# Kernel optimization log

Hardware: AMD Instinct MI355X
Metric: run time of the kernel (lower is better)

## Reference

```python
import jax, jax.numpy as jnp
from jax import lax
import numpy as np

S = 3600  # spatial_size from scn.InputLayer
B = 1     # batch
P = 200000
NEG = jnp.float32(-1e30)


def setup_inputs() -> dict:
    key = jax.random.key(0)
    ks = jax.random.split(key, 10)
    coords = jax.random.randint(ks[0], (P, 2), 0, S, dtype=jnp.int32)
    features = jax.random.normal(ks[1], (P, 1), jnp.float32)
    w1 = jax.random.normal(ks[2], (5, 5, 1, 10), jnp.float32) * 0.2
    w2 = jax.random.normal(ks[3], (5, 5, 10, 64), jnp.float32) * 0.06
    w3 = jax.random.normal(ks[4], (5, 5, 64, 128), jnp.float32) * 0.025
    w4 = jax.random.normal(ks[5], (5, 5, 128, 256), jnp.float32) * 0.018
    fc1_w = jax.random.normal(ks[6], (256 * 9 * 9, 32), jnp.float32) * 0.01
    fc1_b = jax.random.normal(ks[7], (32,), jnp.float32) * 0.01
    fc2_w = jax.random.normal(ks[8], (32, 5), jnp.float32) * 0.1
    fc2_b = jax.random.normal(ks[9], (5,), jnp.float32) * 0.01
    return dict(coords=coords, features=features, w1=w1, w2=w2, w3=w3, w4=w4,
                fc1_w=fc1_w, fc1_b=fc1_b, fc2_w=fc2_w, fc2_b=fc2_b)


def _subm_conv(x, mask, w):
    # Submanifold conv == dense SAME conv on zero-filled grid, output kept
    # only at active sites (inactive inputs are exactly zero by construction).
    y = lax.conv_general_dilated(x, w, (1, 1), 'SAME',
                                 dimension_numbers=('NHWC', 'HWIO', 'NHWC'))
    return y * mask


def _sparse_maxpool(x, mask, k):
    # scn.MaxPooling: max over ACTIVE sites in each window; output site is
    # active iff any input site in the window is active, else feature = 0.
    neg = jnp.where(mask > 0, x, NEG)
    y = lax.reduce_window(neg, NEG, lax.max, (1, k, k, 1), (1, k, k, 1), 'VALID')
    new_mask = lax.reduce_window(mask, jnp.float32(0), lax.max,
                                 (1, k, k, 1), (1, k, k, 1), 'VALID')
    return jnp.where(new_mask > 0, y, 0.0), new_mask


def reference(coords, features, w1, w2, w3, w4, fc1_w, fc1_b, fc2_w, fc2_b):
    # scn.InputLayer: scatter sparse (coord, feature) pairs onto the grid
    x = jnp.zeros((B, S, S, 1), jnp.float32).at[0, coords[:, 0], coords[:, 1], :].add(features)
    mask = jnp.zeros((B, S, S, 1), jnp.float32).at[0, coords[:, 0], coords[:, 1], :].set(1.0)

    x = jax.nn.elu(_subm_conv(x, mask, w1))
    x, mask = _sparse_maxpool(x, mask, 5)   # 3600 -> 720
    x = jax.nn.elu(_subm_conv(x, mask, w2))
    x, mask = _sparse_maxpool(x, mask, 5)   # 720 -> 144
    x = jax.nn.elu(_subm_conv(x, mask, w3))
    x, mask = _sparse_maxpool(x, mask, 4)   # 144 -> 36
    x = jax.nn.elu(_subm_conv(x, mask, w4))
    x, mask = _sparse_maxpool(x, mask, 4)   # 36 -> 9

    # SparseToDense -> (B, 256, 9, 9), then view(-1, 256*9*9) in NCHW order
    h = x.transpose(0, 3, 1, 2).reshape(B, 256 * 9 * 9)
    h = jax.nn.elu(h @ fc1_w + fc1_b)
    logits = h @ fc2_w + fc2_b
    return jax.nn.softmax(logits, axis=1)
```

## Files before the change

### kernel.cpp

```cpp
#include <hip/hip_runtime.h>
#include <math.h>

#define S0 3600
#define S1 720
#define S2 144
#define S3 36
#define S4 9
#define NEGF (-1e30f)

static constexpr size_t OFF_X0  = 0;
static constexpr size_t OFF_M0B = (size_t)S0 * S0 * 4;
static constexpr size_t OFF_H1  = OFF_M0B + 1620000;
static constexpr size_t OFF_Y1H = OFF_H1 + 128;
static constexpr size_t OFF_M1  = OFF_Y1H + (size_t)S1 * S1 * 16 * 2;
static constexpr size_t OFF_M2  = 1330000;
static constexpr size_t OFF_Y3  = OFF_M2 + 20736;
static constexpr size_t OFF_M3  = OFF_Y3 + (size_t)S3 * S3 * 128 * 4;
static constexpr size_t OFF_Y4  = OFF_M3 + 1296;
static constexpr size_t OFF_Y2H = 13000000;
static constexpr size_t OFF_W3H = 18400000;
static constexpr size_t OFF_W2H = 19240000;
static constexpr size_t OFF_W4H = 19400000;

typedef __attribute__((ext_vector_type(8))) short bf16x8;
typedef __attribute__((ext_vector_type(4))) float f32x4;

__device__ __forceinline__ float eluf(float x) { return x > 0.f ? x : expm1f(x); }
__device__ __forceinline__ unsigned short f2bf(float f) {
    unsigned u = __float_as_uint(f);
    unsigned r = u + 0x7FFFu + ((u >> 16) & 1u);
    return (unsigned short)(r >> 16);
}
__device__ __forceinline__ float bf2f(unsigned short h) {
    return __uint_as_float((unsigned)h << 16);
}

__global__ __launch_bounds__(256) void k_zero(const int* __restrict__ coords,
                                              float* __restrict__ x0, int P) {
    int i = blockIdx.x * 256 + threadIdx.x;
    if (i >= P) return;
    x0[coords[2 * i] * S0 + coords[2 * i + 1]] = 0.f;
}

__global__ __launch_bounds__(256) void k_scatter(const int* __restrict__ coords,
                                                 const float* __restrict__ feats,
                                                 float* __restrict__ x0,
                                                 unsigned* __restrict__ m0b, int P) {
    int i = blockIdx.x * 256 + threadIdx.x;
    if (i >= P) return;
    int r = coords[2 * i], c = coords[2 * i + 1];
    int idx = r * S0 + c;
    atomicAdd(&x0[idx], feats[i]);
    atomicOr(&m0b[idx >> 5], 1u << (idx & 31));
}

__global__ __launch_bounds__(256) void k_l1(const float* __restrict__ x0,
                                            const unsigned* __restrict__ m0b,
                                            const float* __restrict__ w1,
                                            unsigned short* __restrict__ y1h,
                                            unsigned char* __restrict__ m1) {
    __shared__ float w1s[250];
    int tid = threadIdx.x;
    if (tid < 250) w1s[tid] = w1[tid];
    __syncthreads();
    int t = blockIdx.x * 256 + tid;
    int pr = t / S1, pc = t % S1;
    int r0 = pr * 5 - 2, c0 = pc * 5 - 2;
    unsigned rows[9];
#pragma unroll
    for (int rr = 0; rr < 9; rr++) {
        unsigned bits = 0;
        int gr = r0 + rr;
        if (gr >= 0 && gr < S0) {
            int cs = c0 < 0 ? 0 : c0;
            int ce = c0 + 8 > S0 - 1 ? S0 - 1 : c0 + 8;
            int span = ce - cs;
            size_t i0 = (size_t)gr * S0 + cs;
            unsigned sh = (unsigned)(i0 & 31);
            unsigned long long two = (unsigned long long)m0b[i0 >> 5] >> sh;
            if ((int)sh + span >= 32)
                two |= (unsigned long long)m0b[(i0 >> 5) + 1] << (32 - sh);
            bits = (unsigned)(two & ((1u << (span + 1)) - 1));
            bits <<= (cs - c0);
        }
        rows[rr] = bits;
    }
    unsigned any25 = 0;
#pragma unroll
    for (int dy = 0; dy < 5; dy++) any25 |= (rows[2 + dy] >> 2) & 0x1Fu;
    uint4* yo = (uint4*)&y1h[(size_t)t * 16];
    if (!any25) {
        yo[0] = make_uint4(0, 0, 0, 0);
        yo[1] = make_uint4(0, 0, 0, 0);
        m1[t] = 0;
        return;
    }
    float2 mx[5];
#pragma unroll
    for (int q = 0; q < 5; q++) mx[q] = make_float2(NEGF, NEGF);
    for (int dy = 0; dy < 5; dy++) {
        unsigned crow = (rows[2 + dy] >> 2) & 0x1Fu;
        while (crow) {
            int dx = __ffs(crow) - 1; crow &= crow - 1;
            float2 acc[5];
#pragma unroll
            for (int q = 0; q < 5; q++) acc[q] = make_float2(0.f, 0.f);
#pragma unroll
            for (int ky = 0; ky < 5; ky++) {
                unsigned nrow = (rows[dy + ky] >> dx) & 0x1Fu;
                size_t rowbase = (size_t)(r0 + dy + ky) * S0 + (c0 + dx);
                while (nrow) {
                    int kx = __ffs(nrow) - 1; nrow &= nrow - 1;
                    float xv = x0[rowbase + kx];
                    const float2* wp = (const float2*)&w1s[(ky * 5 + kx) * 10];
#pragma unroll
                    for (int q = 0; q < 5; q++) {
                        float2 w = wp[q];
                        acc[q].x = fmaf(xv, w.x, acc[q].x);
                        acc[q].y = fmaf(xv, w.y, acc[q].y);
                    }
                }
            }
#pragma unroll
            for (int q = 0; q < 5; q++) {
                mx[q].x = fmaxf(mx[q].x, acc[q].x);
                mx[q].y = fmaxf(mx[q].y, acc[q].y);
            }
        }
    }
    unsigned u[8];
#pragma unroll
    for (int q = 0; q < 5; q++) {
        unsigned short h0 = f2bf(eluf(mx[q].x));
        unsigned short h1 = f2bf(eluf(mx[q].y));
        u[q] = (unsigned)h0 | ((unsigned)h1 << 16);
    }
    u[5] = 0; u[6] = 0; u[7] = 0;
    yo[0] = make_uint4(u[0], u[1], u[2], u[3]);
    yo[1] = make_uint4(u[4], u[5], u[6], u[7]);
    m1[t] = 1;
}

__global__ __launch_bounds__(256) void k_cvtw_all(const float* __restrict__ w2,
                                                  const float* __restrict__ w3,
                                                  const float* __restrict__ w4,
                                                  unsigned short* __restrict__ w2h,
                                                  unsigned short* __restrict__ w3h,
                                                  unsigned short* __restrict__ w4h) {
    int blk = blockIdx.x;
    int tid = threadIdx.x;
    if (blk < 13) {
        int t = blk * 256 + tid;
        int s = t >> 8, rem = t & 255;
        int nt = rem >> 6, lane = rem & 63;
        int quad = lane >> 4, n = lane & 15;
        int tap = 2 * s + (quad >> 1);
#pragma unroll
        for (int j = 0; j < 8; j++) {
            int ci = (quad & 1) * 8 + j;
            float v = 0.f;
            if (tap < 25 && ci < 10) v = w2[(tap * 10 + ci) * 64 + nt * 16 + n];
            w2h[(size_t)t * 8 + j] = f2bf(v);
        }
    } else if (blk < 113) {
        int t = (blk - 13) * 256 + tid;
        int s = t >> 9, rem = t & 511;
        int nt = rem >> 6, lane = rem & 63;
        int quad = lane >> 4, n = lane & 15;
        int t5 = s >> 1, cib = s & 1;
#pragma unroll
        for (int j = 0; j < 8; j++) {
            int ci = cib * 32 + quad * 8 + j;
            float v = w3[(size_t)(t5 * 64 + ci) * 128 + nt * 16 + n];
            w3h[(size_t)t * 8 + j] = f2bf(v);
        }
    } else {
        int t = (blk - 113) * 256 + tid;
        int s = t >> 10, rem = t & 1023;
        int nt = rem >> 6, lane = rem & 63;
        int quad = lane >> 4, n = lane & 15;
        int t5 = s >> 2, cib = s & 3;
#pragma unroll
        for (int j = 0; j < 8; j++) {
            int ci = cib * 32 + quad * 8 + j;
            float v = w4[(size_t)(t5 * 128 + ci) * 256 + nt * 16 + n];
            w4h[(size_t)t * 8 + j] = f2bf(v);
        }
    }
}

__global__ __launch_bounds__(256, 4) void k_l2(const unsigned short* __restrict__ y1h,
                                               const unsigned char* __restrict__ m1,
                                               const unsigned short* __restrict__ w2h,
                                               unsigned short* __restrict__ y2h,
                                               unsigned char* __restrict__ m2) {
    __shared__ unsigned short winh[240 * 16];
    __shared__ unsigned char sm[196];
    int b = blockIdx.x;
    int bpr = b / 72, bpc = b % 72;
    int r0 = bpr * 10 - 2, c0 = bpc * 10 - 2;
    int tid = threadIdx.x;
    if (tid < 240) {
        uint4 v0 = make_uint4(0, 0, 0, 0), v1 = v0;
        if (tid < 196) {
            int gr = r0 + tid / 14, gc = c0 + tid % 14;
            bool ok = (gr >= 0 && gr < S1 && gc >= 0 && gc < S1);
            sm[tid] = ok ? m1[gr * S1 + gc] : (unsigned char)0;
            if (ok) {
                const uint4* src = (const uint4*)&y1h[(size_t)(gr * S1 + gc) * 16];
                v0 = src[0];
                v1 = src[1];
            }
        }
        uint4* dh = (uint4*)&winh[tid * 16];
        dh[0] = v0;
        dh[1] = v1;
    }
    __syncthreads();
    int wv = tid >> 6;
    int a = wv >> 1, bq = wv & 1;
    int lane = tid & 63, quad = lane >> 4, n = lane & 15;
    int cql = lane & 31, s01l = lane >> 5;
    bool pv = false;
    if (cql < 25)
        pv = sm[(a * 5 + 2 + cql / 5) * 14 + s01l * 5 + 2 + cql % 5] != 0;
    unsigned long long bal = __ballot(pv);
    unsigned mb[2];
    mb[0] = (unsigned)(bal & 0x1FFFFFFull);
    mb[1] = (unsigned)((bal >> 32) & 0x1FFFFFFull);
    const bf16x8* wh8 = (const bf16x8*)w2h;
    const bf16x8* xh8 = (const bf16x8*)winh;
    int oct = quad & 1, qh = quad >> 1;
    int base[2][2];
#pragma unroll
    for (int s01 = 0; s01 < 2; s01++)
#pragma unroll
        for (int mt = 0; mt < 2; mt++) {
            int cell = mt * 16 + n;
            base[s01][mt] = ((a * 5 + cell / 5) * 14 + s01 * 5 + cell % 5) * 2 + oct;
        }
    constexpr int TOFF[26] = {0, 1, 2, 3, 4, 14, 15, 16, 17, 18, 28, 29, 30, 31,
                              32, 42, 43, 44, 45, 46, 56, 57, 58, 59, 60, 70};
    f32x4 acc[2][2][2];
#pragma unroll
    for (int s01 = 0; s01 < 2; s01++)
#pragma unroll
        for (int mt = 0; mt < 2; mt++)
#pragma unroll
            for (int ntl = 0; ntl < 2; ntl++) acc[s01][mt][ntl] = (f32x4){0.f, 0.f, 0.f, 0.f};
#pragma unroll
    for (int s = 0; s < 13; s++) {
        int toff2 = 2 * (qh ? TOFF[2 * s + 1] : TOFF[2 * s]);
        bf16x8 ah[2][2];
#pragma unroll
        for (int s01 = 0; s01 < 2; s01++)
#pragma unroll
            for (int mt = 0; mt < 2; mt++) ah[s01][mt] = xh8[base[s01][mt] + toff2];
#pragma unroll
        for (int ntl = 0; ntl < 2; ntl++) {
            bf16x8 bh = wh8[(s * 4 + bq * 2 + ntl) * 64 + lane];
#pragma unroll
            for (int s01 = 0; s01 < 2; s01++)
#pragma unroll
                for (int mt = 0; mt < 2; mt++)
                    acc[s01][mt][ntl] = __builtin_amdgcn_mfma_f32_16x16x32_bf16(ah[s01][mt], bh, acc[s01][mt][ntl], 0, 0, 0);
        }
    }
#pragma unroll
    for (int s01 = 0; s01 < 2; s01++) {
        int gsite = (bpr * 2 + a) * S2 + bpc * 2 + s01;
#pragma unroll
        for (int ntl = 0; ntl < 2; ntl++) {
            float m = NEGF;
#pragma unroll
            for (int mt = 0; mt < 2; mt++) {
#pragma unroll
                for (int r = 0; r < 4; r++) {
                    int cell = mt * 16 + quad * 4 + r;
                    if (cell < 25 && (mb[s01] & (1u << cell))) m = fmaxf(m, acc[s01][mt][ntl][r]);
                }
            }
            m = fmaxf(m, __shfl_xor(m, 16, 64));
            m = fmaxf(m, __shfl_xor(m, 32, 64));
            if (quad == 0) {
                int nt = bq * 2 + ntl;
                y2h[(size_t)gsite * 64 + nt * 16 + n] = mb[s01] ? f2bf(eluf(m)) : (unsigned short)0;
            }
        }
        if (bq == 0 && lane == 0) m2[gsite] = mb[s01] ? 1 : 0;
    }
}

__global__ __launch_bounds__(256) void k_l3(const unsigned short* __restrict__ y2h,
                                            const unsigned char* __restrict__ m2,
                                            const unsigned short* __restrict__ w3h,
                                            float* __restrict__ y3,
                                            unsigned char* __restrict__ m3) {
    __shared__ uint4 win_h4[1152];
    __shared__ unsigned char sm[64];
    int b = blockIdx.x;
    int pr2 = b / 18, pc2 = b % 18;
    int r0 = pr2 * 8 - 2, c0 = pc2 * 8 - 2;
    int tid = threadIdx.x;
    for (int k = tid; k < 1152; k += 256) {
        int cellk = k >> 3, q = k & 7;
        int gr = r0 + cellk / 12, gc = c0 + cellk % 12;
        uint4 vh = make_uint4(0, 0, 0, 0);
        if (gr >= 0 && gr < S2 && gc >= 0 && gc < S2)
            vh = ((const uint4*)y2h)[(size_t)(gr * S2 + gc) * 8 + q];
        win_h4[k] = vh;
    }
    if (tid < 64) sm[tid] = m2[(pr2 * 8 + (tid >> 3)) * S2 + pc2 * 8 + (tid & 7)];
    __syncthreads();
    const bf16x8* winh8 = (const bf16x8*)win_h4;
    const bf16x8* w3h8 = (const bf16x8*)w3h;
    int wv = tid >> 6, lane = tid & 63;
    int quad = lane >> 4, n = lane & 15;
    int cellr = n >> 2, cellc = n & 3;
    f32x4 acc[4][2];
#pragma unroll
    for (int si = 0; si < 4; si++)
#pragma unroll
        for (int ntl = 0; ntl < 2; ntl++) acc[si][ntl] = (f32x4){0.f, 0.f, 0.f, 0.f};
    int bb = (wv * 2) * 64 + lane;
    bf16x8 bh0 = w3h8[bb];
    bf16x8 bh1 = w3h8[bb + 64];
#pragma unroll 2
    for (int s = 0; s < 50; s++) {
        int sp = s + 1 < 50 ? s + 1 : 0;
        int nb = (sp * 8 + wv * 2) * 64 + lane;
        bf16x8 nh0 = w3h8[nb];
        bf16x8 nh1 = w3h8[nb + 64];
        int t5 = s >> 1, cib = s & 1;
        int ky = t5 / 5, kx = t5 % 5;
        int common = ((cellr + ky) * 12 + (cellc + kx)) * 8 + cib * 4 + quad;
#pragma unroll
        for (int si = 0; si < 4; si++) {
            bf16x8 ah = winh8[common + (si >> 1) * 384 + (si & 1) * 32];
            acc[si][0] = __builtin_amdgcn_mfma_f32_16x16x32_bf16(ah, bh0, acc[si][0], 0, 0, 0);
            acc[si][1] = __builtin_amdgcn_mfma_f32_16x16x32_bf16(ah, bh1, acc[si][1], 0, 0, 0);
        }
        bh0 = nh0; bh1 = nh1;
    }
#pragma unroll
    for (int si = 0; si < 4; si++) {
        int srb = (si >> 1) * 4, scb = (si & 1) * 4;
        bool anyv = false;
#pragma unroll
        for (int i = 0; i < 16; i++) anyv |= (sm[(srb + (i >> 2)) * 8 + scb + (i & 3)] != 0);
        int sg = (2 * pr2 + (si >> 1)) * S3 + 2 * pc2 + (si & 1);
#pragma unroll
        for (int ntl = 0; ntl < 2; ntl++) {
            float mv = NEGF;
#pragma unroll
            for (int r = 0; r < 4; r++) {
                int cell = quad * 4 + r;
                if (sm[(srb + (cell >> 2)) * 8 + scb + (cell & 3)]) mv = fmaxf(mv, acc[si][ntl][r]);
            }
            mv = fmaxf(mv, __shfl_xor(mv, 16, 64));
            mv = fmaxf(mv, __shfl_xor(mv, 32, 64));
            if (quad == 0)
                y3[(size_t)sg * 128 + (wv * 2 + ntl) * 16 + n] = anyv ? eluf(mv) : 0.f;
        }
        if (tid == 0) m3[sg] = anyv ? 1 : 0;
    }
}

__global__ __launch_bounds__(1024) void k_l4(const float* __restrict__ y3,
                                             const unsigned char* __restrict__ m3,
                                             const unsigned short* __restrict__ w4h,
                                             float* __restrict__ y4) {
    __shared__ unsigned short winh[64 * 128];
    __shared__ unsigned char sm[16];
    int p = blockIdx.x;
    int ppr = p / S4, ppc = p % S4;
    int r0 = ppr * 4 - 2, c0 = ppc * 4 - 2;
    int tid = threadIdx.x;
    for (int k = tid; k < 2048; k += 1024) {
        int cellk = k >> 5, q = k & 31;
        int gr = r0 + (cellk >> 3), gc = c0 + (cellk & 7);
        float4 v = make_float4(0.f, 0.f, 0.f, 0.f);
        if (gr >= 0 && gr < S3 && gc >= 0 && gc < S3)
            v = ((const float4*)y3)[((size_t)gr * S3 + gc) * 32 + q];
        unsigned short h0 = f2bf(v.x), h1 = f2bf(v.y), h2 = f2bf(v.z), h3 = f2bf(v.w);
        unsigned uh0 = (unsigned)h0 | ((unsigned)h1 << 16);
        unsigned uh1 = (unsigned)h2 | ((unsigned)h3 << 16);
        ((uint2*)winh)[k] = make_uint2(uh0, uh1);
    }
    if (tid < 16) sm[tid] = m3[(ppr * 4 + (tid >> 2)) * S3 + ppc * 4 + (tid & 3)];
    __syncthreads();
    const bf16x8* winh8 = (const bf16x8*)winh;
    const bf16x8* w4h8 = (const bf16x8*)w4h;
    int wv = tid >> 6, lane = tid & 63;
    int quad = lane >> 4, n = lane & 15;
    int cellr = n >> 2, cellc = n & 3;
    f32x4 acc = {0.f, 0.f, 0.f, 0.f};
    int wb = wv * 64 + lane;
    bf16x8 bha = w4h8[wb];
    bf16x8 bhb = w4h8[1024 + wb];
#pragma unroll 2
    for (int s = 0; s < 100; s++) {
        int sp = s + 2 < 100 ? s + 2 : 0;
        bf16x8 nh = w4h8[sp * 1024 + wb];
        int t5 = s >> 2, cib = s & 3;
        int ky = t5 / 5, kx = t5 % 5;
        int aidx = ((cellr + ky) * 8 + (cellc + kx)) * 16 + cib * 4 + quad;
        bf16x8 ah = winh8[aidx];
        acc = __builtin_amdgcn_mfma_f32_16x16x32_bf16(ah, bha, acc, 0, 0, 0);
        bha = bhb; bhb = nh;
    }
    bool anyv = false;
#pragma unroll
    for (int i = 0; i < 16; i++) anyv |= (sm[i] != 0);
    float m = NEGF;
#pragma unroll
    for (int r = 0; r < 4; r++) {
        int cell = quad * 4 + r;
        if (sm[cell]) m = fmaxf(m, acc[r]);
    }
    m = fmaxf(m, __shfl_xor(m, 16, 64));
    m = fmaxf(m, __shfl_xor(m, 32, 64));
    if (quad == 0)
        y4[(size_t)p * 256 + wv * 16 + n] = anyv ? eluf(m) : 0.f;
}

__global__ __launch_bounds__(256) void k_fc1(const float* __restrict__ y4,
                                             const float* __restrict__ fc1_w,
                                             float* __restrict__ h1) {
    __shared__ float wsum[4][32];
    int t = threadIdx.x;
    int i = blockIdx.x * 256 + t;
    int c = i / 81, rem = i % 81;
    float x = y4[(size_t)rem * 256 + c];
    const float4* wr = (const float4*)&fc1_w[(size_t)i * 32];
    float4 w[8];
#pragma unroll
    for (int q = 0; q < 8; q++) w[q] = wr[q];
    int lane = t & 63, wv = t >> 6;
#pragma unroll
    for (int q = 0; q < 8; q++) {
#pragma unroll
        for (int k = 0; k < 4; k++) {
            float v = x * ((&w[q].x)[k]);
            v += __shfl_down(v, 32, 64);
            v += __shfl_down(v, 16, 64);
            v += __shfl_down(v, 8, 64);
            v += __shfl_down(v, 4, 64);
            v += __shfl_down(v, 2, 64);
            v += __shfl_down(v, 1, 64);
            if (lane == 0) wsum[wv][q * 4 + k] = v;
        }
    }
    __syncthreads();
    if (t < 32) {
        float s = wsum[0][t] + wsum[1][t] + wsum[2][t] + wsum[3][t];
        atomicAdd(&h1[t], s);
    }
}

__global__ __launch_bounds__(64) void k_fc2(const float* __restrict__ h1,
                                            const float* __restrict__ fc1_b,
                                            const float* __restrict__ fc2_w,
                                            const float* __restrict__ fc2_b,
                                            float* __restrict__ out) {
    __shared__ float hv[32];
    __shared__ float lg[5];
    int tid = threadIdx.x;
    if (tid < 32) hv[tid] = eluf(h1[tid] + fc1_b[tid]);
    __syncthreads();
    if (tid < 5) {
        float s = fc2_b[tid];
        for (int j = 0; j < 32; j++) s = fmaf(hv[j], fc2_w[j * 5 + tid], s);
        lg[tid] = s;
    }
    __syncthreads();
    if (tid == 0) {
        float m = lg[0];
        for (int k = 1; k < 5; k++) m = fmaxf(m, lg[k]);
        float e[5], sum = 0.f;
        for (int k = 0; k < 5; k++) { e[k] = expf(lg[k] - m); sum += e[k]; }
        for (int k = 0; k < 5; k++) out[k] = e[k] / sum;
    }
}

extern "C" void kernel_launch(void* const* d_in, const int* in_sizes, int n_in,
                              void* d_out, int out_size, void* d_ws, size_t ws_size,
                              hipStream_t stream) {
    const int* coords = (const int*)d_in[0];
    const float* feats = (const float*)d_in[1];
    const float* w1 = (const float*)d_in[2];
    const float* w2 = (const float*)d_in[3];
    const float* w3 = (const float*)d_in[4];
    const float* w4 = (const float*)d_in[5];
    const float* fc1w = (const float*)d_in[6];
    const float* fc1b = (const float*)d_in[7];
    const float* fc2w = (const float*)d_in[8];
    const float* fc2b = (const float*)d_in[9];
    float* out = (float*)d_out;
    char* ws = (char*)d_ws;
    float* x0 = (float*)(ws + OFF_X0);
    unsigned* m0b = (unsigned*)(ws + OFF_M0B);
    unsigned short* y1h = (unsigned short*)(ws + OFF_Y1H);
    unsigned char* m1g = (unsigned char*)(ws + OFF_M1);
    unsigned char* m2g = (unsigned char*)(ws + OFF_M2);
    float* y3 = (float*)(ws + OFF_Y3);
    unsigned char* m3g = (unsigned char*)(ws + OFF_M3);
    float* y4 = (float*)(ws + OFF_Y4);
    float* h1 = (float*)(ws + OFF_H1);
    unsigned short* y2h = (unsigned short*)(ws + OFF_Y2H);
    unsigned short* w3h = (unsigned short*)(ws + OFF_W3H);
    unsigned short* w2h = (unsigned short*)(ws + OFF_W2H);
    unsigned short* w4h = (unsigned short*)(ws + OFF_W4H);
    int P = in_sizes[1];

    hipMemsetAsync(ws + OFF_M0B, 0, 1620000 + 128, stream);
    k_zero<<<(P + 255) / 256, 256, 0, stream>>>(coords, x0, P);
    k_scatter<<<(P + 255) / 256, 256, 0, stream>>>(coords, feats, x0, m0b, P);
    k_l1<<<(S1 * S1) / 256, 256, 0, stream>>>(x0, m0b, w1, y1h, m1g);
    k_cvtw_all<<<513, 256, 0, stream>>>(w2, w3, w4, w2h, w3h, w4h);
    k_l2<<<72 * 72, 256, 0, stream>>>(y1h, m1g, w2h, y2h, m2g);
    k_l3<<<18 * 18, 256, 0, stream>>>(y2h, m2g, w3h, y3, m3g);
    k_l4<<<S4 * S4, 1024, 0, stream>>>(y3, m3g, w4h, y4);
    k_fc1<<<81, 256, 0, stream>>>(y4, fc1w, h1);
    k_fc2<<<1, 64, 0, stream>>>(h1, fc1b, fc2w, fc2b, out);
}
```

Before: 235.7 us.

## Fuse weight conversion into L1, fuse FC kernels, pad LDS strides

```diff
diff --git a/kernel.cpp b/kernel.cpp
--- a/kernel.cpp
+++ b/kernel.cpp
@@ -11,16 +11,17 @@
 static constexpr size_t OFF_X0  = 0;
 static constexpr size_t OFF_M0B = (size_t)S0 * S0 * 4;
 static constexpr size_t OFF_H1  = OFF_M0B + 1620000;
-static constexpr size_t OFF_Y1H = OFF_H1 + 128;
+static constexpr size_t OFF_CNT = OFF_H1 + 128;
+static constexpr size_t OFF_Y1H = OFF_CNT + 32;
 static constexpr size_t OFF_M1  = OFF_Y1H + (size_t)S1 * S1 * 16 * 2;
 static constexpr size_t OFF_M2  = 1330000;
 static constexpr size_t OFF_Y3  = OFF_M2 + 20736;
 static constexpr size_t OFF_M3  = OFF_Y3 + (size_t)S3 * S3 * 128 * 4;
 static constexpr size_t OFF_Y4  = OFF_M3 + 1296;
-static constexpr size_t OFF_Y2H = 13000000;
-static constexpr size_t OFF_W3H = 18400000;
-static constexpr size_t OFF_W2H = 19240000;
-static constexpr size_t OFF_W4H = 19400000;
+static constexpr size_t OFF_Y2H = 80000000;
+static constexpr size_t OFF_W2H = 84000000;
+static constexpr size_t OFF_W3H = 84200000;
+static constexpr size_t OFF_W4H = 84700000;
 
 typedef __attribute__((ext_vector_type(8))) short bf16x8;
 typedef __attribute__((ext_vector_type(4))) float f32x4;
@@ -54,16 +55,65 @@
     atomicOr(&m0b[idx >> 5], 1u << (idx & 31));
 }
 
-__global__ __launch_bounds__(256) void k_l1(const float* __restrict__ x0,
-                                            const unsigned* __restrict__ m0b,
-                                            const float* __restrict__ w1,
-                                            unsigned short* __restrict__ y1h,
-                                            unsigned char* __restrict__ m1) {
+__global__ __launch_bounds__(256) void k_l1c(const float* __restrict__ x0,
+                                             const unsigned* __restrict__ m0b,
+                                             const float* __restrict__ w1,
+                                             const float* __restrict__ w2,
+                                             const float* __restrict__ w3,
+                                             const float* __restrict__ w4,
+                                             unsigned short* __restrict__ y1h,
+                                             unsigned char* __restrict__ m1,
+                                             unsigned short* __restrict__ w2h,
+                                             unsigned short* __restrict__ w3h,
+                                             unsigned short* __restrict__ w4h) {
+    int b = blockIdx.x;
+    int tid = threadIdx.x;
+    if (b >= 2025) {
+        int blk = b - 2025;
+        if (blk < 13) {
+            int t = blk * 256 + tid;
+            int s = t >> 8, rem = t & 255;
+            int nt = rem >> 6, lane = rem & 63;
+            int quad = lane >> 4, n = lane & 15;
+            int tap = 2 * s + (quad >> 1);
+#pragma unroll
+            for (int j = 0; j < 8; j++) {
+                int ci = (quad & 1) * 8 + j;
+                float v = 0.f;
+                if (tap < 25 && ci < 10) v = w2[(tap * 10 + ci) * 64 + nt * 16 + n];
+                w2h[(size_t)t * 8 + j] = f2bf(v);
+            }
+        } else if (blk < 113) {
+            int t = (blk - 13) * 256 + tid;
+            int s = t >> 9, rem = t & 511;
+            int nt = rem >> 6, lane = rem & 63;
+            int quad = lane >> 4, n = lane & 15;
+            int t5 = s >> 1, cib = s & 1;
+#pragma unroll
+            for (int j = 0; j < 8; j++) {
+                int ci = cib * 32 + quad * 8 + j;
+                float v = w3[(size_t)(t5 * 64 + ci) * 128 + nt * 16 + n];
+                w3h[(size_t)t * 8 + j] = f2bf(v);
+            }
+        } else {
+            int t = (blk - 113) * 256 + tid;
+            int s = t >> 10, rem = t & 1023;
+            int nt = rem >> 6, lane = rem & 63;
+            int quad = lane >> 4, n = lane & 15;
+            int t5 = s >> 2, cib = s & 3;
+#pragma unroll
+            for (int j = 0; j < 8; j++) {
+                int ci = cib * 32 + quad * 8 + j;
+                float v = w4[(size_t)(t5 * 128 + ci) * 256 + nt * 16 + n];
+                w4h[(size_t)t * 8 + j] = f2bf(v);
+            }
+        }
+        return;
+    }
     __shared__ float w1s[250];
-    int tid = threadIdx.x;
     if (tid < 250) w1s[tid] = w1[tid];
     __syncthreads();
-    int t = blockIdx.x * 256 + tid;
+    int t = b * 256 + tid;
     int pr = t / S1, pc = t % S1;
     int r0 = pr * 5 - 2, c0 = pc * 5 - 2;
     unsigned rows[9];
@@ -141,60 +191,12 @@
     m1[t] = 1;
 }
 
-__global__ __launch_bounds__(256) void k_cvtw_all(const float* __restrict__ w2,
-                                                  const float* __restrict__ w3,
-                                                  const float* __restrict__ w4,
-                                                  unsigned short* __restrict__ w2h,
-                                                  unsigned short* __restrict__ w3h,
-                                                  unsigned short* __restrict__ w4h) {
-    int blk = blockIdx.x;
-    int tid = threadIdx.x;
-    if (blk < 13) {
-        int t = blk * 256 + tid;
-        int s = t >> 8, rem = t & 255;
-        int nt = rem >> 6, lane = rem & 63;
-        int quad = lane >> 4, n = lane & 15;
-        int tap = 2 * s + (quad >> 1);
-#pragma unroll
-        for (int j = 0; j < 8; j++) {
-            int ci = (quad & 1) * 8 + j;
-            float v = 0.f;
-            if (tap < 25 && ci < 10) v = w2[(tap * 10 + ci) * 64 + nt * 16 + n];
-            w2h[(size_t)t * 8 + j] = f2bf(v);
-        }
-    } else if (blk < 113) {
-        int t = (blk - 13) * 256 + tid;
-        int s = t >> 9, rem = t & 511;
-        int nt = rem >> 6, lane = rem & 63;
-        int quad = lane >> 4, n = lane & 15;
-        int t5 = s >> 1, cib = s & 1;
-#pragma unroll
-        for (int j = 0; j < 8; j++) {
-            int ci = cib * 32 + quad * 8 + j;
-            float v = w3[(size_t)(t5 * 64 + ci) * 128 + nt * 16 + n];
-            w3h[(size_t)t * 8 + j] = f2bf(v);
-        }
-    } else {
-        int t = (blk - 113) * 256 + tid;
-        int s = t >> 10, rem = t & 1023;
-        int nt = rem >> 6, lane = rem & 63;
-        int quad = lane >> 4, n = lane & 15;
-        int t5 = s >> 2, cib = s & 3;
-#pragma unroll
-        for (int j = 0; j < 8; j++) {
-            int ci = cib * 32 + quad * 8 + j;
-            float v = w4[(size_t)(t5 * 128 + ci) * 256 + nt * 16 + n];
-            w4h[(size_t)t * 8 + j] = f2bf(v);
-        }
-    }
-}
-
 __global__ __launch_bounds__(256, 4) void k_l2(const unsigned short* __restrict__ y1h,
                                                const unsigned char* __restrict__ m1,
                                                const unsigned short* __restrict__ w2h,
                                                unsigned short* __restrict__ y2h,
                                                unsigned char* __restrict__ m2) {
-    __shared__ unsigned short winh[240 * 16];
+    __shared__ unsigned short winh[240 * 24];
     __shared__ unsigned char sm[196];
     int b = blockIdx.x;
     int bpr = b / 72, bpc = b % 72;
@@ -212,7 +214,7 @@
                 v1 = src[1];
             }
         }
-        uint4* dh = (uint4*)&winh[tid * 16];
+        uint4* dh = (uint4*)&winh[tid * 24];
         dh[0] = v0;
         dh[1] = v1;
     }
@@ -237,7 +239,7 @@
 #pragma unroll
         for (int mt = 0; mt < 2; mt++) {
             int cell = mt * 16 + n;
-            base[s01][mt] = ((a * 5 + cell / 5) * 14 + s01 * 5 + cell % 5) * 2 + oct;
+            base[s01][mt] = ((a * 5 + cell / 5) * 14 + s01 * 5 + cell % 5) * 3 + oct;
         }
     constexpr int TOFF[26] = {0, 1, 2, 3, 4, 14, 15, 16, 17, 18, 28, 29, 30, 31,
                               32, 42, 43, 44, 45, 46, 56, 57, 58, 59, 60, 70};
@@ -250,12 +252,12 @@
             for (int ntl = 0; ntl < 2; ntl++) acc[s01][mt][ntl] = (f32x4){0.f, 0.f, 0.f, 0.f};
 #pragma unroll
     for (int s = 0; s < 13; s++) {
-        int toff2 = 2 * (qh ? TOFF[2 * s + 1] : TOFF[2 * s]);
+        int toff3 = 3 * (qh ? TOFF[2 * s + 1] : TOFF[2 * s]);
         bf16x8 ah[2][2];
 #pragma unroll
         for (int s01 = 0; s01 < 2; s01++)
 #pragma unroll
-            for (int mt = 0; mt < 2; mt++) ah[s01][mt] = xh8[base[s01][mt] + toff2];
+            for (int mt = 0; mt < 2; mt++) ah[s01][mt] = xh8[base[s01][mt] + toff3];
 #pragma unroll
         for (int ntl = 0; ntl < 2; ntl++) {
             bf16x8 bh = wh8[(s * 4 + bq * 2 + ntl) * 64 + lane];
@@ -296,7 +298,7 @@
                                             const unsigned short* __restrict__ w3h,
                                             float* __restrict__ y3,
                                             unsigned char* __restrict__ m3) {
-    __shared__ uint4 win_h4[1152];
+    __shared__ uint4 win_h4[144 * 9];
     __shared__ unsigned char sm[64];
     int b = blockIdx.x;
     int pr2 = b / 18, pc2 = b % 18;
@@ -308,7 +310,7 @@
         uint4 vh = make_uint4(0, 0, 0, 0);
         if (gr >= 0 && gr < S2 && gc >= 0 && gc < S2)
             vh = ((const uint4*)y2h)[(size_t)(gr * S2 + gc) * 8 + q];
-        win_h4[k] = vh;
+        win_h4[cellk * 9 + q] = vh;
     }
     if (tid < 64) sm[tid] = m2[(pr2 * 8 + (tid >> 3)) * S2 + pc2 * 8 + (tid & 7)];
     __syncthreads();
@@ -333,10 +335,10 @@
         bf16x8 nh1 = w3h8[nb + 64];
         int t5 = s >> 1, cib = s & 1;
         int ky = t5 / 5, kx = t5 % 5;
-        int common = ((cellr + ky) * 12 + (cellc + kx)) * 8 + cib * 4 + quad;
+        int common = ((cellr + ky) * 12 + (cellc + kx)) * 9 + cib * 4 + quad;
 #pragma unroll
         for (int si = 0; si < 4; si++) {
-            bf16x8 ah = winh8[common + (si >> 1) * 384 + (si & 1) * 32];
+            bf16x8 ah = winh8[common + (si >> 1) * 432 + (si & 1) * 36];
             acc[si][0] = __builtin_amdgcn_mfma_f32_16x16x32_bf16(ah, bh0, acc[si][0], 0, 0, 0);
             acc[si][1] = __builtin_amdgcn_mfma_f32_16x16x32_bf16(ah, bh1, acc[si][1], 0, 0, 0);
         }
@@ -370,7 +372,7 @@
                                              const unsigned char* __restrict__ m3,
                                              const unsigned short* __restrict__ w4h,
                                              float* __restrict__ y4) {
-    __shared__ unsigned short winh[64 * 128];
+    __shared__ unsigned short winh[1120 * 8];
     __shared__ unsigned char sm[16];
     int p = blockIdx.x;
     int ppr = p / S4, ppc = p % S4;
@@ -378,14 +380,15 @@
     int tid = threadIdx.x;
     for (int k = tid; k < 2048; k += 1024) {
         int cellk = k >> 5, q = k & 31;
-        int gr = r0 + (cellk >> 3), gc = c0 + (cellk & 7);
+        int cr = cellk >> 3, cc = cellk & 7;
+        int gr = r0 + cr, gc = c0 + cc;
         float4 v = make_float4(0.f, 0.f, 0.f, 0.f);
         if (gr >= 0 && gr < S3 && gc >= 0 && gc < S3)
             v = ((const float4*)y3)[((size_t)gr * S3 + gc) * 32 + q];
         unsigned short h0 = f2bf(v.x), h1 = f2bf(v.y), h2 = f2bf(v.z), h3 = f2bf(v.w);
         unsigned uh0 = (unsigned)h0 | ((unsigned)h1 << 16);
         unsigned uh1 = (unsigned)h2 | ((unsigned)h3 << 16);
-        ((uint2*)winh)[k] = make_uint2(uh0, uh1);
+        ((uint2*)winh)[cr * 280 + cc * 34 + q] = make_uint2(uh0, uh1);
     }
     if (tid < 16) sm[tid] = m3[(ppr * 4 + (tid >> 2)) * S3 + ppc * 4 + (tid & 3)];
     __syncthreads();
@@ -404,7 +407,7 @@
         bf16x8 nh = w4h8[sp * 1024 + wb];
         int t5 = s >> 2, cib = s & 3;
         int ky = t5 / 5, kx = t5 % 5;
-        int aidx = ((cellr + ky) * 8 + (cellc + kx)) * 16 + cib * 4 + quad;
+        int aidx = (cellr + ky) * 140 + (cellc + kx) * 17 + cib * 4 + quad;
         bf16x8 ah = winh8[aidx];
         acc = __builtin_amdgcn_mfma_f32_16x16x32_bf16(ah, bha, acc, 0, 0, 0);
         bha = bhb; bhb = nh;
@@ -424,10 +427,18 @@
         y4[(size_t)p * 256 + wv * 16 + n] = anyv ? eluf(m) : 0.f;
 }
 
-__global__ __launch_bounds__(256) void k_fc1(const float* __restrict__ y4,
-                                             const float* __restrict__ fc1_w,
-                                             float* __restrict__ h1) {
+__global__ __launch_bounds__(256) void k_fc(const float* __restrict__ y4,
+                                            const float* __restrict__ fc1_w,
+                                            const float* __restrict__ fc1_b,
+                                            const float* __restrict__ fc2_w,
+                                            const float* __restrict__ fc2_b,
+                                            float* __restrict__ h1,
+                                            unsigned* __restrict__ cnt,
+                                            float* __restrict__ out) {
     __shared__ float wsum[4][32];
+    __shared__ int lastflag;
+    __shared__ float hv[32];
+    __shared__ float lg[5];
     int t = threadIdx.x;
     int i = blockIdx.x * 256 + t;
     int c = i / 81, rem = i % 81;
@@ -456,25 +467,20 @@
         float s = wsum[0][t] + wsum[1][t] + wsum[2][t] + wsum[3][t];
         atomicAdd(&h1[t], s);
     }
-}
-
-__global__ __launch_bounds__(64) void k_fc2(const float* __restrict__ h1,
-                                            const float* __restrict__ fc1_b,
-                                            const float* __restrict__ fc2_w,
-                                            const float* __restrict__ fc2_b,
-                                            float* __restrict__ out) {
-    __shared__ float hv[32];
-    __shared__ float lg[5];
-    int tid = threadIdx.x;
-    if (tid < 32) hv[tid] = eluf(h1[tid] + fc1_b[tid]);
-    __syncthreads();
-    if (tid < 5) {
-        float s = fc2_b[tid];
-        for (int j = 0; j < 32; j++) s = fmaf(hv[j], fc2_w[j * 5 + tid], s);
-        lg[tid] = s;
-    }
-    __syncthreads();
-    if (tid == 0) {
+    __threadfence();
+    __syncthreads();
+    if (t == 0) lastflag = (atomicAdd(cnt, 1u) == 80u) ? 1 : 0;
+    __syncthreads();
+    if (!lastflag) return;
+    if (t < 32) hv[t] = eluf(atomicAdd(&h1[t], 0.f) + fc1_b[t]);
+    __syncthreads();
+    if (t < 5) {
+        float s = fc2_b[t];
+        for (int j = 0; j < 32; j++) s = fmaf(hv[j], fc2_w[j * 5 + t], s);
+        lg[t] = s;
+    }
+    __syncthreads();
+    if (t == 0) {
         float m = lg[0];
         for (int k = 1; k < 5; k++) m = fmaxf(m, lg[k]);
         float e[5], sum = 0.f;
@@ -507,20 +513,20 @@
     unsigned char* m3g = (unsigned char*)(ws + OFF_M3);
     float* y4 = (float*)(ws + OFF_Y4);
     float* h1 = (float*)(ws + OFF_H1);
+    unsigned* cnt = (unsigned*)(ws + OFF_CNT);
     unsigned short* y2h = (unsigned short*)(ws + OFF_Y2H);
+    unsigned short* w2h = (unsigned short*)(ws + OFF_W2H);
     unsigned short* w3h = (unsigned short*)(ws + OFF_W3H);
-    unsigned short* w2h = (unsigned short*)(ws + OFF_W2H);
     unsigned short* w4h = (unsigned short*)(ws + OFF_W4H);
     int P = in_sizes[1];
 
-    hipMemsetAsync(ws + OFF_M0B, 0, 1620000 + 128, stream);
+    hipMemsetAsync(ws + OFF_M0B, 0, 1620000 + 160, stream);
     k_zero<<<(P + 255) / 256, 256, 0, stream>>>(coords, x0, P);
     k_scatter<<<(P + 255) / 256, 256, 0, stream>>>(coords, feats, x0, m0b, P);
-    k_l1<<<(S1 * S1) / 256, 256, 0, stream>>>(x0, m0b, w1, y1h, m1g);
-    k_cvtw_all<<<513, 256, 0, stream>>>(w2, w3, w4, w2h, w3h, w4h);
+    k_l1c<<<2025 + 513, 256, 0, stream>>>(x0, m0b, w1, w2, w3, w4,
+                                          y1h, m1g, w2h, w3h, w4h);
     k_l2<<<72 * 72, 256, 0, stream>>>(y1h, m1g, w2h, y2h, m2g);
     k_l3<<<18 * 18, 256, 0, stream>>>(y2h, m2g, w3h, y3, m3g);
     k_l4<<<S4 * S4, 1024, 0, stream>>>(y3, m3g, w4h, y4);
-    k_fc1<<<81, 256, 0, stream>>>(y4, fc1w, h1);
-    k_fc2<<<1, 64, 0, stream>>>(h1, fc1b, fc2w, fc2b, out);
-}
+    k_fc<<<81, 256, 0, stream>>>(y4, fc1w, fc1b, fc2w, fc2b, h1, cnt, out);
+}
```

Measured after the change: 227.2 us. -3.6%, faster.
